# Kernel optimization log

Hardware: AMD Instinct MI355X
Metric: run time of the kernel (lower is better)

Reference implementation:

```python
import jax, jax.numpy as jnp
import numpy as np

N, D, K, R_DIM = 20000, 256, 16, 64
RADIUS = 50.0     # init radius
ALPHA = 2.0       # hardcoded in forward
THRESH = 0.01     # attention_threshold
EPS_LN = 1e-5     # torch LayerNorm default eps


def layer_norm(v, g, b):
    m = jnp.mean(v, axis=-1, keepdims=True)
    var = jnp.mean((v - m) ** 2, axis=-1, keepdims=True)
    return (v - m) / jnp.sqrt(var + EPS_LN) * g + b


def setup_inputs() -> dict:
    key = jax.random.key(0)
    ks = jax.random.split(key, 8)
    x = jax.random.normal(ks[0], (N, D), dtype=jnp.float32)
    # fixed-degree graph: node i has exactly K neighbors
    row = jnp.repeat(jnp.arange(N, dtype=jnp.int32), K)
    col = jax.random.randint(ks[1], (N * K,), 0, N, dtype=jnp.int32)
    edge_index = jnp.stack([row, col], axis=0)
    spatial_coords = jax.random.uniform(ks[2], (N, 2), dtype=jnp.float32) * 100.0
    gamma = jnp.ones((D,), jnp.float32)
    beta_ln = jnp.zeros((D,), jnp.float32)
    W_self = jax.random.normal(ks[3], (D, D), jnp.float32) * 0.05
    b_self = jnp.zeros((D,), jnp.float32)
    W_nei = jax.random.normal(ks[4], (D, D), jnp.float32) * 0.05
    b_nei = jnp.zeros((D,), jnp.float32)
    W_red = jax.random.normal(ks[5], (R_DIM, D), jnp.float32) * 0.05
    b_red = jnp.zeros((R_DIM,), jnp.float32)
    beta_mix = jnp.asarray(0.5, jnp.float32)
    return {"x": x, "spatial_coords": spatial_coords, "gamma": gamma,
            "beta_ln": beta_ln, "W_self": W_self, "b_self": b_self,
            "W_nei": W_nei, "b_nei": b_nei, "W_red": W_red, "b_red": b_red,
            "beta_mix": beta_mix, "edge_index": edge_index}


def reference(x, spatial_coords, gamma, beta_ln, W_self, b_self, W_nei, b_nei,
              W_red, b_red, beta_mix, edge_index):
    col = edge_index[1].reshape(N, K)              # fixed degree K per node
    neighbors = x[col]                             # [N, K, D] gather
    nb_coords = spatial_coords[col]                # [N, K, 2]
    distances = jnp.linalg.norm(spatial_coords[:, None, :] - nb_coords, axis=-1)  # [N, K]

    t = layer_norm(x, gamma, beta_ln)              # [N, D]
    nb = layer_norm(neighbors, gamma, beta_ln)     # [N, K, D]

    s_scores = t @ W_self.T + b_self               # [N, D]
    n_scores = nb @ W_nei.T + b_nei                # [N, K, D]

    dist_w = jnp.exp(-ALPHA * distances / (RADIUS + 1e-8))  # [N, K]
    weighted_n = n_scores * dist_w[..., None]

    combined = jnp.concatenate([s_scores[:, None, :], weighted_n], axis=1)  # [N, K+1, D]
    cw = jax.nn.softmax(combined, axis=1)
    self_w = cw[:, 0, :]
    nb_w = cw[:, 1:, :]
    self_w = jnp.where(jnp.abs(self_w) >= THRESH, self_w, 0.0)
    nb_w = jnp.where(jnp.abs(nb_w) >= THRESH, nb_w, 0.0)

    context = beta_mix * (self_w * t) + (1.0 - beta_mix) * jnp.sum(nb_w * nb, axis=1)
    reduced = jax.nn.leaky_relu(context @ W_red.T + b_red, 0.01)
    # outer forward applies leaky_relu again (dropout is identity in eval)
    return jax.nn.leaky_relu(reduced, 0.01)
```

## Files before the change

kernel.cpp:

```cpp
#include <hip/hip_runtime.h>
#include <cmath>

#define NN 20000
#define DD 256
#define KK 16

typedef __attribute__((ext_vector_type(8))) short short8;
typedef __attribute__((ext_vector_type(4))) float f32x4;
typedef unsigned int u32;
typedef unsigned short bfu;

__device__ __forceinline__ float b2f(bfu u) {
  union { u32 i; float f; } v; v.i = ((u32)u) << 16; return v.f;
}
__device__ __forceinline__ bfu f2b(float f) {
  u32 u = __float_as_uint(f);
  u = (u + 0x7fff + ((u >> 16) & 1)) >> 16;
  return (bfu)u;
}
__device__ __forceinline__ float wave_sum(float v) {
#pragma unroll
  for (int m = 32; m; m >>= 1) v += __shfl_xor(v, m, 64);
  return v;
}
__device__ __forceinline__ void gl_lds16(const void* g, void* l) {
  __builtin_amdgcn_global_load_lds((const __attribute__((address_space(1))) u32*)g,
                                   (__attribute__((address_space(3))) u32*)l, 16, 0, 0);
}

__global__ __launch_bounds__(256) void conv_kernel(
    const float* __restrict__ Wself, const float* __restrict__ Wnei,
    const float* __restrict__ Wred, bfu* __restrict__ Wcat, bfu* __restrict__ Wredb) {
  int idx = blockIdx.x * 256 + threadIdx.x;
  if (idx < 65536) Wcat[idx] = f2b(Wself[idx]);
  else if (idx < 131072) Wcat[idx] = f2b(Wnei[idx - 65536]);
  else Wredb[idx - 131072] = f2b(Wred[idx - 131072]);
}

__global__ __launch_bounds__(256) void ln_kernel(
    const float* __restrict__ x, const float* __restrict__ g,
    const float* __restrict__ b, bfu* __restrict__ t) {
  int lane = threadIdx.x & 63;
  int row = (blockIdx.x << 2) + (threadIdx.x >> 6);
  float4 v = ((const float4*)(x + (size_t)row * DD))[lane];
  float mean = wave_sum(v.x + v.y + v.z + v.w) * (1.0f / 256.0f);
  float4 d = make_float4(v.x - mean, v.y - mean, v.z - mean, v.w - mean);
  float var = wave_sum(d.x * d.x + d.y * d.y + d.z * d.z + d.w * d.w) * (1.0f / 256.0f);
  float rstd = 1.0f / sqrtf(var + 1e-5f);
  float4 g4 = ((const float4*)g)[lane];
  float4 b4 = ((const float4*)b)[lane];
  bfu* o = t + (size_t)row * DD + (lane << 2);
  ushort4 ov;
  ov.x = f2b(d.x * rstd * g4.x + b4.x);
  ov.y = f2b(d.y * rstd * g4.y + b4.y);
  ov.z = f2b(d.z * rstd * g4.z + b4.z);
  ov.w = f2b(d.w * rstd * g4.w + b4.w);
  *(ushort4*)o = ov;
}

template<int NT, bool FINAL>
__global__ __launch_bounds__(256) void gemm_kernel(
    const bfu* __restrict__ A, const bfu* __restrict__ Bw,
    const float* __restrict__ bias0, const float* __restrict__ bias1,
    void* __restrict__ Cout, int ldc, int M) {
  constexpr int FM = (NT == 128) ? 4 : 2;
  constexpr int WM = (NT == 128) ? 64 : 32;
  constexpr int ASLOTS = 1024;
  constexpr int BSLOTS = NT * 8;
  __shared__ bfu smA[128 * 64];
  __shared__ bfu smB[NT * 64];
  int tid = threadIdx.x;
  int lane = tid & 63;
  int wid = tid >> 6;
  int m0 = blockIdx.x * 128;
  int nbase = blockIdx.y * NT;
  const bfu* Bt = Bw + (size_t)nbase * 256;
  int wr = (NT == 128) ? (wid >> 1) : wid;
  int wc = (NT == 128) ? (wid & 1) : 0;

  f32x4 acc[FM][4];
#pragma unroll
  for (int i = 0; i < FM; ++i)
#pragma unroll
    for (int j = 0; j < 4; ++j) acc[i][j] = (f32x4){0.f, 0.f, 0.f, 0.f};

  int lr = lane & 15, lk = lane >> 4;

  for (int kc = 0; kc < 256; kc += 64) {
    __syncthreads();
#pragma unroll
    for (int i = 0; i < ASLOTS / 256; ++i) {
      int p = tid + 256 * i;
      int row = p >> 3;
      int c = (p & 7) ^ (row & 7);
      gl_lds16(A + (size_t)(m0 + row) * 256 + kc + c * 8, smA + p * 8);
    }
#pragma unroll
    for (int i = 0; i < BSLOTS / 256; ++i) {
      int p = tid + 256 * i;
      int row = p >> 3;
      int c = (p & 7) ^ (row & 7);
      gl_lds16(Bt + (size_t)row * 256 + kc + c * 8, smB + p * 8);
    }
    __syncthreads();

#pragma unroll
    for (int h = 0; h < 2; ++h) {
      short8 af[FM], bfr[4];
      int cc = h * 4 + lk;
#pragma unroll
      for (int fm = 0; fm < FM; ++fm) {
        int row = wr * WM + fm * 16 + lr;
        af[fm] = *(const short8*)(smA + row * 64 + ((cc ^ (row & 7)) << 3));
      }
#pragma unroll
      for (int fn = 0; fn < 4; ++fn) {
        int row = wc * 64 + fn * 16 + lr;
        bfr[fn] = *(const short8*)(smB + row * 64 + ((cc ^ (row & 7)) << 3));
      }
#pragma unroll
      for (int fm = 0; fm < FM; ++fm)
#pragma unroll
        for (int fn = 0; fn < 4; ++fn)
          acc[fm][fn] = __builtin_amdgcn_mfma_f32_16x16x32_bf16(af[fm], bfr[fn], acc[fm][fn], 0, 0, 0);
    }
  }

  const float* bias = (nbase < 256) ? (bias0 + nbase) : (bias1 + (nbase - 256));
#pragma unroll
  for (int fm = 0; fm < FM; ++fm) {
#pragma unroll
    for (int fn = 0; fn < 4; ++fn) {
      int lc = wc * 64 + fn * 16 + lr;
      float bv = bias[lc];
      int gc = nbase + lc;
#pragma unroll
      for (int r = 0; r < 4; ++r) {
        int grow = m0 + wr * WM + fm * 16 + lk * 4 + r;
        if (grow < M) {
          float val = acc[fm][fn][r] + bv;
          if (FINAL) {
            val = (val > 0.f) ? val : 0.01f * val;
            val = (val > 0.f) ? val : 0.01f * val;
            ((float*)Cout)[(size_t)grow * ldc + gc] = val;
          } else {
            ((bfu*)Cout)[(size_t)grow * ldc + gc] = f2b(val);
          }
        }
      }
    }
  }
}

__global__ __launch_bounds__(256) void gather_kernel(
    const bfu* __restrict__ Csu, const bfu* __restrict__ t,
    const float* __restrict__ coords, const int* __restrict__ col,
    const float* __restrict__ bmix, bfu* __restrict__ ctx) {
  int lane = threadIdx.x & 63;
  int i = (blockIdx.x << 2) + (threadIdx.x >> 6);
  float beta = bmix[0];

  int ck = col[i * KK + (lane & 15)];
  float2 ci = ((const float2*)coords)[i];
  float2 cn = ((const float2*)coords)[ck];
  float dx = ci.x - cn.x, dy = ci.y - cn.y;
  float dwv = __expf((-2.0f / (50.0f + 1e-8f)) * sqrtf(dx * dx + dy * dy));

  int d = lane << 2;
  ushort4 sv = *(const ushort4*)(Csu + (size_t)i * 512 + d);
  float4 e0 = make_float4(__expf(b2f(sv.x)), __expf(b2f(sv.y)),
                          __expf(b2f(sv.z)), __expf(b2f(sv.w)));
  float4 Z = e0;
  float4 u4[KK];
#pragma unroll
  for (int k = 0; k < KK; ++k) {
    int cc = __shfl(ck, k, 64);
    float w = __shfl(dwv, k, 64);
    ushort4 uv = *(const ushort4*)(Csu + (size_t)cc * 512 + 256 + d);
    float4 e = make_float4(__expf(w * b2f(uv.x)), __expf(w * b2f(uv.y)),
                           __expf(w * b2f(uv.z)), __expf(w * b2f(uv.w)));
    u4[k] = e;
    Z.x += e.x; Z.y += e.y; Z.z += e.z; Z.w += e.w;
  }
  float4 inv = make_float4(1.f / Z.x, 1.f / Z.y, 1.f / Z.z, 1.f / Z.w);

  ushort4 tv = *(const ushort4*)(t + (size_t)i * DD + d);
  float w0x = e0.x * inv.x; w0x = (w0x >= 0.01f) ? w0x : 0.f;
  float w0y = e0.y * inv.y; w0y = (w0y >= 0.01f) ? w0y : 0.f;
  float w0z = e0.z * inv.z; w0z = (w0z >= 0.01f) ? w0z : 0.f;
  float w0w = e0.w * inv.w; w0w = (w0w >= 0.01f) ? w0w : 0.f;

  float4 ns = make_float4(0.f, 0.f, 0.f, 0.f);
#pragma unroll
  for (int k = 0; k < KK; ++k) {
    int cc = __shfl(ck, k, 64);
    ushort4 tn = *(const ushort4*)(t + (size_t)cc * DD + d);
    float wx = u4[k].x * inv.x; wx = (wx >= 0.01f) ? wx : 0.f;
    float wy = u4[k].y * inv.y; wy = (wy >= 0.01f) ? wy : 0.f;
    float wz = u4[k].z * inv.z; wz = (wz >= 0.01f) ? wz : 0.f;
    float ww = u4[k].w * inv.w; ww = (ww >= 0.01f) ? ww : 0.f;
    ns.x += wx * b2f(tn.x); ns.y += wy * b2f(tn.y);
    ns.z += wz * b2f(tn.z); ns.w += ww * b2f(tn.w);
  }
  float ob = 1.0f - beta;
  ushort4 ov;
  ov.x = f2b(beta * w0x * b2f(tv.x) + ob * ns.x);
  ov.y = f2b(beta * w0y * b2f(tv.y) + ob * ns.y);
  ov.z = f2b(beta * w0z * b2f(tv.z) + ob * ns.z);
  ov.w = f2b(beta * w0w * b2f(tv.w) + ob * ns.w);
  *(ushort4*)(ctx + (size_t)i * DD + d) = ov;
}

extern "C" void kernel_launch(void* const* d_in, const int* in_sizes, int n_in,
                              void* d_out, int out_size, void* d_ws, size_t ws_size,
                              hipStream_t stream) {
  (void)in_sizes; (void)n_in; (void)out_size; (void)ws_size;
  const float* x       = (const float*)d_in[0];
  const float* coords  = (const float*)d_in[1];
  const float* gamma   = (const float*)d_in[2];
  const float* beta_ln = (const float*)d_in[3];
  const float* W_self  = (const float*)d_in[4];
  const float* b_self  = (const float*)d_in[5];
  const float* W_nei   = (const float*)d_in[6];
  const float* b_nei   = (const float*)d_in[7];
  const float* W_red   = (const float*)d_in[8];
  const float* b_red   = (const float*)d_in[9];
  const float* bmix    = (const float*)d_in[10];
  const int*   edge    = (const int*)d_in[11];
  const int*   col     = edge + (size_t)NN * KK;

  bfu* t_b   = (bfu*)d_ws;
  bfu* Csu_b = (bfu*)((char*)d_ws + 10240000);
  bfu* ctx_b = (bfu*)((char*)d_ws + 30720000);
  bfu* Wcat  = (bfu*)((char*)d_ws + 40960000);
  bfu* Wredb = (bfu*)((char*)d_ws + 41222144);

  conv_kernel<<<576, 256, 0, stream>>>(W_self, W_nei, W_red, Wcat, Wredb);
  ln_kernel<<<5000, 256, 0, stream>>>(x, gamma, beta_ln, t_b);
  gemm_kernel<128, false><<<dim3(157, 4), 256, 0, stream>>>(
      t_b, Wcat, b_self, b_nei, (void*)Csu_b, 512, NN);
  gather_kernel<<<5000, 256, 0, stream>>>(Csu_b, t_b, coords, col, bmix, ctx_b);
  gemm_kernel<64, true><<<dim3(157, 1), 256, 0, stream>>>(
      ctx_b, Wredb, b_red, b_red, d_out, 64, NN);
}
```

Before: 159.5 us.

## Interleave LN output with scores, double-buffer GEMM, fuse prep kernels, defer softmax normalization

Merges the weight conversion and layer-norm kernels into one launch, and writes the normalized rows into a combined 768-wide buffer next to the self and neighbor scores. Each neighbor gather then reads scores and normalized features from the same row. The GEMM now double-buffers its LDS tiles so global-to-LDS loads overlap with MFMA. Its operands are swapped so each lane writes four contiguous output columns as one vector store. The gather uses exp2, compares against a scaled threshold instead of dividing per weight, and divides once at the end; it trades more registers for earlier loads and a larger strided layout.

```diff
diff --git a/kernel.cpp b/kernel.cpp
--- a/kernel.cpp
+++ b/kernel.cpp
@@ -4,6 +4,7 @@
 #define NN 20000
 #define DD 256
 #define KK 16
+#define LDC3 768
 
 typedef __attribute__((ext_vector_type(8))) short short8;
 typedef __attribute__((ext_vector_type(4))) float f32x4;
@@ -28,55 +29,54 @@
                                    (__attribute__((address_space(3))) u32*)l, 16, 0, 0);
 }
 
-__global__ __launch_bounds__(256) void conv_kernel(
-    const float* __restrict__ Wself, const float* __restrict__ Wnei,
-    const float* __restrict__ Wred, bfu* __restrict__ Wcat, bfu* __restrict__ Wredb) {
-  int idx = blockIdx.x * 256 + threadIdx.x;
-  if (idx < 65536) Wcat[idx] = f2b(Wself[idx]);
-  else if (idx < 131072) Wcat[idx] = f2b(Wnei[idx - 65536]);
-  else Wredb[idx - 131072] = f2b(Wred[idx - 131072]);
-}
-
-__global__ __launch_bounds__(256) void ln_kernel(
+__global__ __launch_bounds__(256) void prep_kernel(
     const float* __restrict__ x, const float* __restrict__ g,
-    const float* __restrict__ b, bfu* __restrict__ t) {
-  int lane = threadIdx.x & 63;
-  int row = (blockIdx.x << 2) + (threadIdx.x >> 6);
-  float4 v = ((const float4*)(x + (size_t)row * DD))[lane];
-  float mean = wave_sum(v.x + v.y + v.z + v.w) * (1.0f / 256.0f);
-  float4 d = make_float4(v.x - mean, v.y - mean, v.z - mean, v.w - mean);
-  float var = wave_sum(d.x * d.x + d.y * d.y + d.z * d.z + d.w * d.w) * (1.0f / 256.0f);
-  float rstd = 1.0f / sqrtf(var + 1e-5f);
-  float4 g4 = ((const float4*)g)[lane];
-  float4 b4 = ((const float4*)b)[lane];
-  bfu* o = t + (size_t)row * DD + (lane << 2);
-  ushort4 ov;
-  ov.x = f2b(d.x * rstd * g4.x + b4.x);
-  ov.y = f2b(d.y * rstd * g4.y + b4.y);
-  ov.z = f2b(d.z * rstd * g4.z + b4.z);
-  ov.w = f2b(d.w * rstd * g4.w + b4.w);
-  *(ushort4*)o = ov;
+    const float* __restrict__ b, const float* __restrict__ Wself,
+    const float* __restrict__ Wnei, const float* __restrict__ Wred,
+    bfu* __restrict__ C3, bfu* __restrict__ Wcat, bfu* __restrict__ Wredb) {
+  int bid = blockIdx.x;
+  if (bid < 5000) {
+    int lane = threadIdx.x & 63;
+    int row = (bid << 2) + (threadIdx.x >> 6);
+    float4 v = ((const float4*)(x + (size_t)row * DD))[lane];
+    float mean = wave_sum(v.x + v.y + v.z + v.w) * (1.0f / 256.0f);
+    float4 d = make_float4(v.x - mean, v.y - mean, v.z - mean, v.w - mean);
+    float var = wave_sum(d.x * d.x + d.y * d.y + d.z * d.z + d.w * d.w) * (1.0f / 256.0f);
+    float rstd = 1.0f / sqrtf(var + 1e-5f);
+    float4 g4 = ((const float4*)g)[lane];
+    float4 b4 = ((const float4*)b)[lane];
+    ushort4 ov;
+    ov.x = f2b(d.x * rstd * g4.x + b4.x);
+    ov.y = f2b(d.y * rstd * g4.y + b4.y);
+    ov.z = f2b(d.z * rstd * g4.z + b4.z);
+    ov.w = f2b(d.w * rstd * g4.w + b4.w);
+    *(ushort4*)(C3 + (size_t)row * LDC3 + 512 + (lane << 2)) = ov;
+  } else {
+    int idx = (bid - 5000) * 256 + threadIdx.x;
+    if (idx < 65536) Wcat[idx] = f2b(Wself[idx]);
+    else if (idx < 131072) Wcat[idx] = f2b(Wnei[idx - 65536]);
+    else if (idx < 147456) Wredb[idx - 131072] = f2b(Wred[idx - 131072]);
+  }
 }
 
 template<int NT, bool FINAL>
 __global__ __launch_bounds__(256) void gemm_kernel(
-    const bfu* __restrict__ A, const bfu* __restrict__ Bw,
+    const bfu* __restrict__ A, int lda, const bfu* __restrict__ Bw,
     const float* __restrict__ bias0, const float* __restrict__ bias1,
     void* __restrict__ Cout, int ldc, int M) {
   constexpr int FM = (NT == 128) ? 4 : 2;
   constexpr int WM = (NT == 128) ? 64 : 32;
-  constexpr int ASLOTS = 1024;
-  constexpr int BSLOTS = NT * 8;
-  __shared__ bfu smA[128 * 64];
-  __shared__ bfu smB[NT * 64];
-  int tid = threadIdx.x;
-  int lane = tid & 63;
-  int wid = tid >> 6;
+  constexpr int AIT = 4;
+  constexpr int BIT = NT / 32;
+  __shared__ bfu smA[2][128 * 64];
+  __shared__ bfu smB[2][NT * 64];
+  int tid = threadIdx.x, lane = tid & 63, wid = tid >> 6;
   int m0 = blockIdx.x * 128;
   int nbase = blockIdx.y * NT;
   const bfu* Bt = Bw + (size_t)nbase * 256;
   int wr = (NT == 128) ? (wid >> 1) : wid;
   int wc = (NT == 128) ? (wid & 1) : 0;
+  int lr = lane & 15, lk = lane >> 4;
 
   f32x4 acc[FM][4];
 #pragma unroll
@@ -84,78 +84,86 @@
 #pragma unroll
     for (int j = 0; j < 4; ++j) acc[i][j] = (f32x4){0.f, 0.f, 0.f, 0.f};
 
-  int lr = lane & 15, lk = lane >> 4;
-
-  for (int kc = 0; kc < 256; kc += 64) {
-    __syncthreads();
-#pragma unroll
-    for (int i = 0; i < ASLOTS / 256; ++i) {
-      int p = tid + 256 * i;
-      int row = p >> 3;
-      int c = (p & 7) ^ (row & 7);
-      gl_lds16(A + (size_t)(m0 + row) * 256 + kc + c * 8, smA + p * 8);
-    }
-#pragma unroll
-    for (int i = 0; i < BSLOTS / 256; ++i) {
-      int p = tid + 256 * i;
-      int row = p >> 3;
-      int c = (p & 7) ^ (row & 7);
-      gl_lds16(Bt + (size_t)row * 256 + kc + c * 8, smB + p * 8);
-    }
-    __syncthreads();
-
-#pragma unroll
-    for (int h = 0; h < 2; ++h) {
-      short8 af[FM], bfr[4];
-      int cc = h * 4 + lk;
-#pragma unroll
-      for (int fm = 0; fm < FM; ++fm) {
-        int row = wr * WM + fm * 16 + lr;
-        af[fm] = *(const short8*)(smA + row * 64 + ((cc ^ (row & 7)) << 3));
-      }
-#pragma unroll
-      for (int fn = 0; fn < 4; ++fn) {
-        int row = wc * 64 + fn * 16 + lr;
-        bfr[fn] = *(const short8*)(smB + row * 64 + ((cc ^ (row & 7)) << 3));
-      }
-#pragma unroll
-      for (int fm = 0; fm < FM; ++fm)
-#pragma unroll
-        for (int fn = 0; fn < 4; ++fn)
-          acc[fm][fn] = __builtin_amdgcn_mfma_f32_16x16x32_bf16(af[fm], bfr[fn], acc[fm][fn], 0, 0, 0);
-    }
-  }
+#define STAGE(buf, kc)                                                          \
+  {                                                                             \
+    _Pragma("unroll") for (int i = 0; i < AIT; ++i) {                           \
+      int p = tid + 256 * i; int row = p >> 3; int c = (p & 7) ^ (row & 7);     \
+      gl_lds16(A + (size_t)(m0 + row) * lda + (kc) + c * 8, &smA[buf][p * 8]);  \
+    }                                                                           \
+    _Pragma("unroll") for (int i = 0; i < BIT; ++i) {                           \
+      int p = tid + 256 * i; int row = p >> 3; int c = (p & 7) ^ (row & 7);     \
+      gl_lds16(Bt + (size_t)row * 256 + (kc) + c * 8, &smB[buf][p * 8]);        \
+    }                                                                           \
+  }
+
+#define COMPUTE(buf)                                                            \
+  {                                                                             \
+    _Pragma("unroll") for (int h = 0; h < 2; ++h) {                             \
+      short8 af[FM], bfr[4];                                                    \
+      int cc = h * 4 + lk;                                                      \
+      _Pragma("unroll") for (int fm = 0; fm < FM; ++fm) {                       \
+        int row = wr * WM + fm * 16 + lr;                                       \
+        af[fm] = *(const short8*)&smA[buf][row * 64 + ((cc ^ (row & 7)) << 3)]; \
+      }                                                                         \
+      _Pragma("unroll") for (int fn = 0; fn < 4; ++fn) {                        \
+        int row = wc * 64 + fn * 16 + lr;                                       \
+        bfr[fn] = *(const short8*)&smB[buf][row * 64 + ((cc ^ (row & 7)) << 3)];\
+      }                                                                         \
+      _Pragma("unroll") for (int fm = 0; fm < FM; ++fm)                         \
+        _Pragma("unroll") for (int fn = 0; fn < 4; ++fn)                        \
+          acc[fm][fn] = __builtin_amdgcn_mfma_f32_16x16x32_bf16(                \
+              bfr[fn], af[fm], acc[fm][fn], 0, 0, 0);                           \
+    }                                                                           \
+  }
+
+  STAGE(0, 0);
+  __syncthreads();
+  STAGE(1, 64);
+  COMPUTE(0);
+  __syncthreads();
+  STAGE(0, 128);
+  COMPUTE(1);
+  __syncthreads();
+  STAGE(1, 192);
+  COMPUTE(0);
+  __syncthreads();
+  COMPUTE(1);
+#undef STAGE
+#undef COMPUTE
 
   const float* bias = (nbase < 256) ? (bias0 + nbase) : (bias1 + (nbase - 256));
 #pragma unroll
   for (int fm = 0; fm < FM; ++fm) {
+    int m = m0 + wr * WM + fm * 16 + lr;
+    if (m >= M) continue;
 #pragma unroll
     for (int fn = 0; fn < 4; ++fn) {
-      int lc = wc * 64 + fn * 16 + lr;
-      float bv = bias[lc];
-      int gc = nbase + lc;
-#pragma unroll
-      for (int r = 0; r < 4; ++r) {
-        int grow = m0 + wr * WM + fm * 16 + lk * 4 + r;
-        if (grow < M) {
-          float val = acc[fm][fn][r] + bv;
-          if (FINAL) {
-            val = (val > 0.f) ? val : 0.01f * val;
-            val = (val > 0.f) ? val : 0.01f * val;
-            ((float*)Cout)[(size_t)grow * ldc + gc] = val;
-          } else {
-            ((bfu*)Cout)[(size_t)grow * ldc + gc] = f2b(val);
-          }
-        }
+      int lc = wc * 64 + fn * 16 + lk * 4;
+      float4 bv = *(const float4*)(bias + lc);
+      float o0 = acc[fm][fn][0] + bv.x;
+      float o1 = acc[fm][fn][1] + bv.y;
+      float o2 = acc[fm][fn][2] + bv.z;
+      float o3 = acc[fm][fn][3] + bv.w;
+      if (FINAL) {
+        o0 = (o0 > 0.f) ? o0 : 0.01f * o0; o0 = (o0 > 0.f) ? o0 : 0.01f * o0;
+        o1 = (o1 > 0.f) ? o1 : 0.01f * o1; o1 = (o1 > 0.f) ? o1 : 0.01f * o1;
+        o2 = (o2 > 0.f) ? o2 : 0.01f * o2; o2 = (o2 > 0.f) ? o2 : 0.01f * o2;
+        o3 = (o3 > 0.f) ? o3 : 0.01f * o3; o3 = (o3 > 0.f) ? o3 : 0.01f * o3;
+        *(float4*)((float*)Cout + (size_t)m * ldc + nbase + lc) =
+            make_float4(o0, o1, o2, o3);
+      } else {
+        ushort4 ov; ov.x = f2b(o0); ov.y = f2b(o1); ov.z = f2b(o2); ov.w = f2b(o3);
+        *(ushort4*)((bfu*)Cout + (size_t)m * ldc + nbase + lc) = ov;
       }
     }
   }
 }
 
 __global__ __launch_bounds__(256) void gather_kernel(
-    const bfu* __restrict__ Csu, const bfu* __restrict__ t,
-    const float* __restrict__ coords, const int* __restrict__ col,
-    const float* __restrict__ bmix, bfu* __restrict__ ctx) {
+    const bfu* __restrict__ C3, const float* __restrict__ coords,
+    const int* __restrict__ col, const float* __restrict__ bmix,
+    bfu* __restrict__ ctx) {
+  const float L2E = 1.4426950408889634f;
   int lane = threadIdx.x & 63;
   int i = (blockIdx.x << 2) + (threadIdx.x >> 6);
   float beta = bmix[0];
@@ -164,50 +172,50 @@
   float2 ci = ((const float2*)coords)[i];
   float2 cn = ((const float2*)coords)[ck];
   float dx = ci.x - cn.x, dy = ci.y - cn.y;
-  float dwv = __expf((-2.0f / (50.0f + 1e-8f)) * sqrtf(dx * dx + dy * dy));
+  float dwv = exp2f((-2.0f * L2E / (50.0f + 1e-8f)) * sqrtf(dx * dx + dy * dy)) * L2E;
 
   int d = lane << 2;
-  ushort4 sv = *(const ushort4*)(Csu + (size_t)i * 512 + d);
-  float4 e0 = make_float4(__expf(b2f(sv.x)), __expf(b2f(sv.y)),
-                          __expf(b2f(sv.z)), __expf(b2f(sv.w)));
+  const bfu* rowi = C3 + (size_t)i * LDC3;
+  ushort4 sv = *(const ushort4*)(rowi + d);
+  float4 e0 = make_float4(exp2f(L2E * b2f(sv.x)), exp2f(L2E * b2f(sv.y)),
+                          exp2f(L2E * b2f(sv.z)), exp2f(L2E * b2f(sv.w)));
   float4 Z = e0;
-  float4 u4[KK];
+  float4 ef[KK];
+  ushort4 tn[KK];
 #pragma unroll
   for (int k = 0; k < KK; ++k) {
     int cc = __shfl(ck, k, 64);
     float w = __shfl(dwv, k, 64);
-    ushort4 uv = *(const ushort4*)(Csu + (size_t)cc * 512 + 256 + d);
-    float4 e = make_float4(__expf(w * b2f(uv.x)), __expf(w * b2f(uv.y)),
-                           __expf(w * b2f(uv.z)), __expf(w * b2f(uv.w)));
-    u4[k] = e;
+    const bfu* rowc = C3 + (size_t)cc * LDC3;
+    ushort4 uv = *(const ushort4*)(rowc + 256 + d);
+    tn[k] = *(const ushort4*)(rowc + 512 + d);
+    float4 e = make_float4(exp2f(w * b2f(uv.x)), exp2f(w * b2f(uv.y)),
+                           exp2f(w * b2f(uv.z)), exp2f(w * b2f(uv.w)));
+    ef[k] = e;
     Z.x += e.x; Z.y += e.y; Z.z += e.z; Z.w += e.w;
   }
-  float4 inv = make_float4(1.f / Z.x, 1.f / Z.y, 1.f / Z.z, 1.f / Z.w);
-
-  ushort4 tv = *(const ushort4*)(t + (size_t)i * DD + d);
-  float w0x = e0.x * inv.x; w0x = (w0x >= 0.01f) ? w0x : 0.f;
-  float w0y = e0.y * inv.y; w0y = (w0y >= 0.01f) ? w0y : 0.f;
-  float w0z = e0.z * inv.z; w0z = (w0z >= 0.01f) ? w0z : 0.f;
-  float w0w = e0.w * inv.w; w0w = (w0w >= 0.01f) ? w0w : 0.f;
-
+  float4 thr = make_float4(0.01f * Z.x, 0.01f * Z.y, 0.01f * Z.z, 0.01f * Z.w);
+  ushort4 tv = *(const ushort4*)(rowi + 512 + d);
+  float ob = 1.0f - beta;
   float4 ns = make_float4(0.f, 0.f, 0.f, 0.f);
 #pragma unroll
   for (int k = 0; k < KK; ++k) {
-    int cc = __shfl(ck, k, 64);
-    ushort4 tn = *(const ushort4*)(t + (size_t)cc * DD + d);
-    float wx = u4[k].x * inv.x; wx = (wx >= 0.01f) ? wx : 0.f;
-    float wy = u4[k].y * inv.y; wy = (wy >= 0.01f) ? wy : 0.f;
-    float wz = u4[k].z * inv.z; wz = (wz >= 0.01f) ? wz : 0.f;
-    float ww = u4[k].w * inv.w; ww = (ww >= 0.01f) ? ww : 0.f;
-    ns.x += wx * b2f(tn.x); ns.y += wy * b2f(tn.y);
-    ns.z += wz * b2f(tn.z); ns.w += ww * b2f(tn.w);
-  }
-  float ob = 1.0f - beta;
+    float ex = (ef[k].x >= thr.x) ? ef[k].x : 0.f;
+    float ey = (ef[k].y >= thr.y) ? ef[k].y : 0.f;
+    float ez = (ef[k].z >= thr.z) ? ef[k].z : 0.f;
+    float ew = (ef[k].w >= thr.w) ? ef[k].w : 0.f;
+    ns.x += ex * b2f(tn[k].x); ns.y += ey * b2f(tn[k].y);
+    ns.z += ez * b2f(tn[k].z); ns.w += ew * b2f(tn[k].w);
+  }
+  float s0x = (e0.x >= thr.x) ? e0.x : 0.f;
+  float s0y = (e0.y >= thr.y) ? e0.y : 0.f;
+  float s0z = (e0.z >= thr.z) ? e0.z : 0.f;
+  float s0w = (e0.w >= thr.w) ? e0.w : 0.f;
   ushort4 ov;
-  ov.x = f2b(beta * w0x * b2f(tv.x) + ob * ns.x);
-  ov.y = f2b(beta * w0y * b2f(tv.y) + ob * ns.y);
-  ov.z = f2b(beta * w0z * b2f(tv.z) + ob * ns.z);
-  ov.w = f2b(beta * w0w * b2f(tv.w) + ob * ns.w);
+  ov.x = f2b((beta * s0x * b2f(tv.x) + ob * ns.x) / Z.x);
+  ov.y = f2b((beta * s0y * b2f(tv.y) + ob * ns.y) / Z.y);
+  ov.z = f2b((beta * s0z * b2f(tv.z) + ob * ns.z) / Z.z);
+  ov.w = f2b((beta * s0w * b2f(tv.w) + ob * ns.w) / Z.w);
   *(ushort4*)(ctx + (size_t)i * DD + d) = ov;
 }
 
@@ -229,17 +237,16 @@
   const int*   edge    = (const int*)d_in[11];
   const int*   col     = edge + (size_t)NN * KK;
 
-  bfu* t_b   = (bfu*)d_ws;
-  bfu* Csu_b = (bfu*)((char*)d_ws + 10240000);
-  bfu* ctx_b = (bfu*)((char*)d_ws + 30720000);
-  bfu* Wcat  = (bfu*)((char*)d_ws + 40960000);
-  bfu* Wredb = (bfu*)((char*)d_ws + 41222144);
-
-  conv_kernel<<<576, 256, 0, stream>>>(W_self, W_nei, W_red, Wcat, Wredb);
-  ln_kernel<<<5000, 256, 0, stream>>>(x, gamma, beta_ln, t_b);
+  bfu* C3    = (bfu*)d_ws;
+  bfu* ctx   = (bfu*)((char*)d_ws + 30867456);
+  bfu* Wcat  = (bfu*)((char*)d_ws + 41156608);
+  bfu* Wredb = (bfu*)((char*)d_ws + 41418752);
+
+  prep_kernel<<<5577, 256, 0, stream>>>(x, gamma, beta_ln, W_self, W_nei, W_red,
+                                        C3, Wcat, Wredb);
   gemm_kernel<128, false><<<dim3(157, 4), 256, 0, stream>>>(
-      t_b, Wcat, b_self, b_nei, (void*)Csu_b, 512, NN);
-  gather_kernel<<<5000, 256, 0, stream>>>(Csu_b, t_b, coords, col, bmix, ctx_b);
+      C3 + 512, LDC3, Wcat, b_self, b_nei, (void*)C3, LDC3, NN);
+  gather_kernel<<<5000, 256, 0, stream>>>(C3, coords, col, bmix, ctx);
   gemm_kernel<64, true><<<dim3(157, 1), 256, 0, stream>>>(
-      ctx_b, Wredb, b_red, b_red, d_out, 64, NN);
-}
+      ctx, DD, Wredb, b_red, b_red, d_out, 64, NN);
+}
```

Result: no change. 159.8 us (+0.2%).
